# Optimization experiments

Hardware: AMD Instinct MI355X
Metric: run time of the kernel (lower is better)

The kernel has to match this reference:

```python
import math
import jax
import jax.numpy as jnp
import numpy as np
from jax import lax

B, IC, OC, K, STYLE_DIM, H, W = 16, 512, 512, 3, 512, 32, 32
EPS = 1e-8


def _blur_kernel():
    # make_kernel([1,3,3,1]) outer product, normalized, times upsample_factor**2 (=4)
    k = jnp.array([1.0, 3.0, 3.0, 1.0], dtype=jnp.float32)
    k2 = k[None, :] * k[:, None]
    k2 = k2 / k2.sum()
    return k2 * 4.0  # [4,4]


def setup_inputs() -> dict:
    key = jax.random.key(0)
    k1, k2, k3, k4 = jax.random.split(key, 4)
    return {
        "input": jax.random.normal(k1, (B, IC, H, W), dtype=jnp.float32),
        "style": jax.random.normal(k2, (B, STYLE_DIM), dtype=jnp.float32),
        "weight": jax.random.normal(k3, (1, OC, IC, K, K), dtype=jnp.float32),
        "mod_weight": jax.random.normal(k4, (IC, STYLE_DIM), dtype=jnp.float32),
        "mod_bias": jnp.ones((IC,), dtype=jnp.float32),  # bias_init=1
    }


def reference(input, style, weight, mod_weight, mod_bias):
    batch, in_ch, h, w_sp = input.shape
    out_ch, ksz = weight.shape[1], weight.shape[3]

    # EqualLinear modulation: scale = 1/sqrt(style_dim), lr_mul=1, no activation
    mod_scale = 1.0 / math.sqrt(mod_weight.shape[1])
    s = style @ (mod_weight * mod_scale).T + mod_bias  # [B, IC]

    # modulate + demodulate
    conv_scale = 1.0 / math.sqrt(in_ch * ksz * ksz)
    wmod = conv_scale * weight * s[:, None, :, None, None]  # [B, OC, IC, K, K]
    demod = lax.rsqrt(jnp.sum(wmod * wmod, axis=(2, 3, 4)) + EPS)  # [B, OC]
    wmod = wmod * demod[:, :, None, None, None]

    # conv_transpose2d(stride=2, padding=0, groups=batch) == per-sample conv with
    # lhs_dilation=2, full padding (K-1), spatially flipped kernel in OIHW layout.
    w_conv = wmod[:, :, :, ::-1, ::-1]  # [B, OC, IC, K, K]

    def one_sample(x, wk):
        # x: [IC, H, W], wk: [OC, IC, K, K] -> [OC, 2H+K-2+1, ...] (65x65 here)
        return lax.conv_general_dilated(
            x[None], wk, window_strides=(1, 1),
            padding=[(ksz - 1, ksz - 1)] * 2,
            lhs_dilation=(2, 2),
            dimension_numbers=("NCHW", "OIHW", "NCHW"))[0]

    out = jax.vmap(one_sample)(input, w_conv)  # [B, OC, 65, 65]

    # Blur: upfirdn2d(up=1, down=1, pad=(1,1)) with symmetric 4x4 kernel -> depthwise conv
    bk = _blur_kernel()
    out = jnp.pad(out, ((0, 0), (0, 0), (1, 1), (1, 1)))
    dk = jnp.tile(bk[None, None], (out_ch, 1, 1, 1))  # [OC, 1, 4, 4]
    out = lax.conv_general_dilated(
        out, dk, window_strides=(1, 1), padding="VALID",
        feature_group_count=out_ch,
        dimension_numbers=("NCHW", "OIHW", "NCHW"))  # [B, OC, 64, 64]
    return out
```

## Files before the change

kernel.cpp:

```cpp
#include <hip/hip_runtime.h>
#include <stdint.h>

typedef unsigned int uint32;
typedef unsigned short u16;
typedef short short8 __attribute__((ext_vector_type(8)));
typedef float floatx4 __attribute__((ext_vector_type(4)));

#define OFF_S      0u
#define OFF_DS     32768u
#define OFF_WSUM   65536u
#define OFF_WPACK  1114112u
#define OFF_XST    5832704u
#define OFF_U      22609920u

__device__ __forceinline__ u16 f2bf(float x){
    uint32 u = __float_as_uint(x);
    uint32 r = (u + 0x7FFFu + ((u>>16)&1u)) >> 16;
    return (u16)r;
}
__device__ __forceinline__ float bf2f(u16 h){
    return __uint_as_float(((uint32)h)<<16);
}

#define GLL16(gp, lp) \
    __builtin_amdgcn_global_load_lds( \
        (const __attribute__((address_space(1))) void*)(gp), \
        (__attribute__((address_space(3))) void*)(lp), 16, 0, 0)

__global__ __launch_bounds__(256) void k_style(const float* __restrict__ style,
                                               const float* __restrict__ mw,
                                               const float* __restrict__ mb,
                                               float* __restrict__ s){
    int gid = blockIdx.x*4 + (threadIdx.x>>6);
    int lane = threadIdx.x & 63;
    int b = gid>>9, ic = gid & 511;
    const float* sp = style + b*512;
    const float* wp = mw + (size_t)ic*512;
    float acc = 0.f;
    for (int d=lane; d<512; d+=64) acc += sp[d]*wp[d];
    for (int off=32; off; off>>=1) acc += __shfl_down(acc, off, 64);
    if (lane==0) s[b*512+ic] = acc*0.044194173824159216f + mb[ic];
}

__global__ __launch_bounds__(256) void k_wprep(const float* __restrict__ w,
                                               float* __restrict__ wsum,
                                               u16* __restrict__ wp){
    int idx = blockIdx.x*256 + threadIdx.x;
    const float* p = w + (size_t)idx*9;
    float vv[9]; float a = 0.f;
    #pragma unroll
    for (int t=0;t<9;++t){ float v=p[t]; vv[t]=v; a += v*v; }
    wsum[idx] = a;
    #pragma unroll
    for (int t=0;t<9;++t) wp[(size_t)t*262144 + idx] = f2bf(vv[t]);
}

__global__ __launch_bounds__(256) void k_dscale(const float* __restrict__ s,
                                                const float* __restrict__ wsum,
                                                float* __restrict__ ds){
    int gid = blockIdx.x*4 + (threadIdx.x>>6);
    int lane = threadIdx.x & 63;
    int b = gid>>9, oc = gid & 511;
    const float* sp = s + b*512;
    const float* wp = wsum + (size_t)oc*512;
    float acc=0.f;
    for (int d=lane; d<512; d+=64){ float sv = sp[d]; acc += sv*sv*wp[d]; }
    for (int off=32; off; off>>=1) acc += __shfl_down(acc, off, 64);
    if (lane==0){
        const float cs = 0.014731391274719738f;
        ds[b*512+oc] = cs * rsqrtf(cs*cs*acc + 1e-8f);
    }
}

__global__ __launch_bounds__(256) void k_xst(const float* __restrict__ in,
                                             const float* __restrict__ s,
                                             u16* __restrict__ xst){
    int bx = blockIdx.x;
    int b = bx>>5, i = bx&31;
    __shared__ u16 tr[32*520];
    int tid = threadIdx.x;
    int j = tid & 31;
    for (int ic = tid>>5; ic < 512; ic += 8){
        float v = in[((size_t)(b*512+ic)*32 + i)*32 + j] * s[b*512+ic];
        tr[j*520 + ic] = f2bf(v);
    }
    __syncthreads();
    for (int v = tid; v < 2048; v += 256){
        int jj = v>>6, ic8 = (v&63)*8;
        *(uint4*)(xst + (size_t)(b*1024 + i*32 + jj)*512 + ic8) =
            *(const uint4*)(&tr[jj*520 + ic8]);
    }
}

__global__ __launch_bounds__(512, 2) void k_gemm(const u16* __restrict__ A,
                                                 const u16* __restrict__ Bx,
                                                 u16* __restrict__ C,
                                                 int Ncols){
    int cpx = gridDim.x >> 3;
    int bid = blockIdx.x;
    int swz = (bid & 7)*cpx + (bid >> 3);
    int bx = swz / 18;
    int by = swz - bx*18;
    int m0 = by*256, n0 = bx*256;

    int tid = threadIdx.x;
    int lane = tid & 63;
    int w  = tid >> 6;
    int wm = w >> 2, wn = w & 3;
    int np = lane & 15, qq = lane >> 4;

    __shared__ __align__(16) char smem[131072];

    int c1 = tid,      r1 = c1 >> 2, s1 = c1 & 3, g1 = s1 ^ ((r1 >> 1) & 3);
    int c2 = tid + 512, r2 = c2 >> 2, s2 = c2 & 3, g2 = s2 ^ ((r2 >> 1) & 3);
    const u16* srcA1 = A  + (size_t)(m0 + r1)*512 + g1*8;
    const u16* srcA2 = A  + (size_t)(m0 + r2)*512 + g2*8;
    const u16* srcB1 = Bx + (size_t)(n0 + r1)*512 + g1*8;
    const u16* srcB2 = Bx + (size_t)(n0 + r2)*512 + g2*8;
    int offA1 = (tid & ~63)*8;
    int offA2 = offA1 + 4096;

    #define STAGE(T) do{ \
        u16* _b = (u16*)smem + ((T)&3)*16384; \
        GLL16(srcA1 + (size_t)(T)*32, _b + offA1); \
        GLL16(srcA2 + (size_t)(T)*32, _b + offA2); \
        GLL16(srcB1 + (size_t)(T)*32, _b + 8192 + offA1); \
        GLL16(srcB2 + (size_t)(T)*32, _b + 8192 + offA2); \
    }while(0)

    int sA = (qq ^ ((np >> 1) & 3)) * 8;
    int pAoff = (wm*128 + np)*32 + sA;
    int pBoff = (wn*64  + np)*32 + sA;

    floatx4 acc[8][4] = {};

    STAGE(0); STAGE(1); STAGE(2);
    asm volatile("s_waitcnt vmcnt(8)" ::: "memory");
    __builtin_amdgcn_s_barrier();

    #pragma unroll
    for (int t = 0; t < 16; ++t){
        const u16* base = (const u16*)smem + (t & 3)*16384;
        short8 af[8], bfr[4];
        #pragma unroll
        for (int mf = 0; mf < 8; ++mf)
            af[mf] = *(const short8*)(base + pAoff + mf*512);
        #pragma unroll
        for (int nf = 0; nf < 4; ++nf)
            bfr[nf] = *(const short8*)(base + 8192 + pBoff + nf*512);

        if (t < 13) STAGE(t+3);

        __builtin_amdgcn_s_setprio(1);
        #pragma unroll
        for (int mf = 0; mf < 8; ++mf)
            #pragma unroll
            for (int nf = 0; nf < 4; ++nf)
                acc[mf][nf] = __builtin_amdgcn_mfma_f32_16x16x32_bf16(
                    af[mf], bfr[nf], acc[mf][nf], 0,0,0);
        __builtin_amdgcn_s_setprio(0);

        if      (t < 13)  asm volatile("s_waitcnt vmcnt(8)" ::: "memory");
        else if (t == 13) asm volatile("s_waitcnt vmcnt(4)" ::: "memory");
        else if (t == 14) asm volatile("s_waitcnt vmcnt(0)" ::: "memory");
        __builtin_amdgcn_s_barrier();
    }
    #undef STAGE

    u16* Csm = (u16*)smem;
    #pragma unroll
    for (int mf = 0; mf < 8; ++mf){
        int row0 = wm*128 + mf*16 + qq*4;
        #pragma unroll
        for (int nf = 0; nf < 4; ++nf){
            int col = wn*64 + nf*16 + np;
            #pragma unroll
            for (int reg = 0; reg < 4; ++reg)
                Csm[(row0+reg)*256 + col] = f2bf(acc[mf][nf][reg]);
        }
    }
    __syncthreads();
    #pragma unroll
    for (int i = 0; i < 16; ++i){
        int c = tid + i*512;
        int row = c >> 5, cc = c & 31;
        uint4 v = *(const uint4*)(&Csm[row*256 + cc*8]);
        *(uint4*)(C + (size_t)(m0+row)*Ncols + n0 + cc*8) = v;
    }
}

__global__ __launch_bounds__(256) void k_blur2(const u16* __restrict__ U,
                                               const float* __restrict__ ds,
                                               float* __restrict__ out,
                                               int b0, int Ncols){
    int oc = blockIdx.x;
    int bp = blockIdx.y;
    int b  = b0 + bp;
    __shared__ __align__(16) u16 Usm[9*1024];
    __shared__ __align__(16) u16 HRsm[3*32*64];
    int tid = threadIdx.x;

    const u16* src0 = U + (size_t)oc*Ncols + (size_t)bp*1024;
    size_t tapstride = (size_t)512 * Ncols;
    #pragma unroll
    for (int it = 0; it < 5; ++it){
        int i = tid + it*256;
        if (i < 1152){
            int tap = i>>7, c8 = i & 127;
            *(uint4*)(&Usm[tap*1024 + c8*8]) =
                *(const uint4*)(src0 + tap*tapstride + c8*8);
        }
    }
    __syncthreads();

    #pragma unroll
    for (int it = 0; it < 12; ++it){
        int task = tid + it*256;
        int a = task >> 10, rem = task & 1023;
        int i = rem >> 5, u = rem & 31;
        const u16* base = Usm + a*3072 + i*32;
        float u0  = bf2f(base[u]);
        float u1  = bf2f(base[1024 + u]);
        float u2  = bf2f(base[2048 + u]);
        float u0p = (u < 31) ? bf2f(base[u + 1])        : 0.f;
        float u1m = (u > 0)  ? bf2f(base[1024 + u - 1]) : 0.f;
        float u1p = (u < 31) ? bf2f(base[1024 + u + 1]) : 0.f;
        float u2m = (u > 0)  ? bf2f(base[2048 + u - 1]) : 0.f;
        float HRe = u1m + 3.f*(u0 + u2m + u1) + u0p + u2;
        float HRo = u0 + u2m + 3.f*(u1 + u0p + u2) + u1p;
        uint32 packed = (uint32)f2bf(HRe) | ((uint32)f2bf(HRo) << 16);
        *(uint32*)(&HRsm[(a*32 + i)*64 + 2*u]) = packed;
    }
    __syncthreads();

    float dsc = ds[b*512 + oc] * (1.f/16.f);
    float* op = out + (size_t)(b*512 + oc) * 4096;
    #pragma unroll
    for (int it = 0; it < 4; ++it){
        int task = tid + it*256;
        int Y = task >> 4, X0 = (task & 15) * 4;
        float o0=0.f,o1=0.f,o2=0.f,o3=0.f;
        int v = Y >> 1;
        #define ACCROW(aa, ii, ww) do{ \
            int _i = (ii); \
            if ((unsigned)_i < 32u){ \
                uint2 rv = *(const uint2*)(&HRsm[((aa)*32 + _i)*64 + X0]); \
                o0 += (ww)*__uint_as_float((rv.x & 0xffffu) << 16); \
                o1 += (ww)*__uint_as_float(rv.x & 0xffff0000u); \
                o2 += (ww)*__uint_as_float((rv.y & 0xffffu) << 16); \
                o3 += (ww)*__uint_as_float(rv.y & 0xffff0000u); \
            } }while(0)
        if ((Y & 1) == 0){
            ACCROW(1, v-1, 1.f);
            ACCROW(0, v,   3.f);
            ACCROW(2, v-1, 3.f);
            ACCROW(1, v,   3.f);
            ACCROW(0, v+1, 1.f);
            ACCROW(2, v,   1.f);
        } else {
            ACCROW(0, v,   1.f);
            ACCROW(2, v-1, 1.f);
            ACCROW(1, v,   3.f);
            ACCROW(0, v+1, 3.f);
            ACCROW(2, v,   3.f);
            ACCROW(1, v+1, 1.f);
        }
        #undef ACCROW
        float4 res = make_float4(dsc*o0, dsc*o1, dsc*o2, dsc*o3);
        *(float4*)(op + Y*64 + X0) = res;
    }
}

extern "C" void kernel_launch(void* const* d_in, const int* in_sizes, int n_in,
                              void* d_out, int out_size, void* d_ws, size_t ws_size,
                              hipStream_t stream){
    const float* input  = (const float*)d_in[0];
    const float* style  = (const float*)d_in[1];
    const float* weight = (const float*)d_in[2];
    const float* mw     = (const float*)d_in[3];
    const float* mb     = (const float*)d_in[4];
    float* out = (float*)d_out;
    char* ws = (char*)d_ws;
    float* s     = (float*)(ws + OFF_S);
    float* ds    = (float*)(ws + OFF_DS);
    float* wsum  = (float*)(ws + OFF_WSUM);
    u16*   wpack = (u16*)(ws + OFF_WPACK);
    u16*   xst   = (u16*)(ws + OFF_XST);
    u16*   U     = (u16*)(ws + OFF_U);

    int NB;
    if      (ws_size >= (size_t)OFF_U + (size_t)4608*16384*2) NB = 16;
    else if (ws_size >= (size_t)OFF_U + (size_t)4608*8192*2)  NB = 8;
    else                                                       NB = 4;
    int npass = 16 / NB;
    int Ncols = NB * 1024;
    int nTilesN = Ncols / 256;

    k_style <<<2048, 256, 0, stream>>>(style, mw, mb, s);
    k_wprep <<<1024, 256, 0, stream>>>(weight, wsum, wpack);
    k_dscale<<<2048, 256, 0, stream>>>(s, wsum, ds);
    k_xst   <<<512,  256, 0, stream>>>(input, s, xst);

    for (int p = 0; p < npass; ++p){
        const u16* xp = xst + (size_t)p * NB * 1024 * 512;
        k_gemm <<<dim3(18*nTilesN), 512, 0, stream>>>(wpack, xp, U, Ncols);
        k_blur2<<<dim3(512, NB),       256, 0, stream>>>(U, ds, out, p*NB, Ncols);
    }
}
```

Baseline: 338.2 us.

## Rework LDS swizzle for GEMM tiles and pack epilogue rows into 32-bit stores

Changes the shared-memory layout of the staged A/B tiles to a row-pair XOR swizzle over 8 slots, so fragment reads and async global-to-LDS writes avoid bank conflicts. Moves the next-stage prefetch ahead of the fragment loads, so global loads are issued earlier in each iteration. Rewrites the epilogue to pack pairs of rows into 32-bit LDS words with a rotating column offset, then unpacks them into two 8-byte global stores per chunk. The aim is lower LDS conflict stalls; the cost is more index arithmetic and narrower global stores in the epilogue.

```diff
diff --git a/kernel.cpp b/kernel.cpp
--- a/kernel.cpp
+++ b/kernel.cpp
@@ -111,12 +111,14 @@
 
     __shared__ __align__(16) char smem[131072];
 
-    int c1 = tid,      r1 = c1 >> 2, s1 = c1 & 3, g1 = s1 ^ ((r1 >> 1) & 3);
-    int c2 = tid + 512, r2 = c2 >> 2, s2 = c2 & 3, g2 = s2 ^ ((r2 >> 1) & 3);
+    int rp1 = tid >> 3, sl1 = tid & 7;
+    int v1 = sl1 ^ (rp1 & 7);
+    int r1 = rp1*2 + ((v1 >> 2) & 1);
+    int g1 = v1 & 3;
     const u16* srcA1 = A  + (size_t)(m0 + r1)*512 + g1*8;
-    const u16* srcA2 = A  + (size_t)(m0 + r2)*512 + g2*8;
+    const u16* srcA2 = srcA1 + (size_t)128*512;
     const u16* srcB1 = Bx + (size_t)(n0 + r1)*512 + g1*8;
-    const u16* srcB2 = Bx + (size_t)(n0 + r2)*512 + g2*8;
+    const u16* srcB2 = srcB1 + (size_t)128*512;
     int offA1 = (tid & ~63)*8;
     int offA2 = offA1 + 4096;
 
@@ -128,9 +130,10 @@
         GLL16(srcB2 + (size_t)(T)*32, _b + 8192 + offA2); \
     }while(0)
 
-    int sA = (qq ^ ((np >> 1) & 3)) * 8;
-    int pAoff = (wm*128 + np)*32 + sA;
-    int pBoff = (wn*64  + np)*32 + sA;
+    int rpn = np >> 1;
+    int slA = ((qq + ((np & 1) << 2)) ^ rpn) << 3;
+    int pAoff = (wm*64 + rpn)*64 + slA;
+    int pBoff = (wn*32 + rpn)*64 + slA;
 
     floatx4 acc[8][4] = {};
 
@@ -140,6 +143,8 @@
 
     #pragma unroll
     for (int t = 0; t < 16; ++t){
+        if (t < 13) STAGE(t+3);
+
         const u16* base = (const u16*)smem + (t & 3)*16384;
         short8 af[8], bfr[4];
         #pragma unroll
@@ -149,8 +154,6 @@
         for (int nf = 0; nf < 4; ++nf)
             bfr[nf] = *(const short8*)(base + 8192 + pBoff + nf*512);
 
-        if (t < 13) STAGE(t+3);
-
         __builtin_amdgcn_s_setprio(1);
         #pragma unroll
         for (int mf = 0; mf < 8; ++mf)
@@ -167,25 +170,37 @@
     }
     #undef STAGE
 
-    u16* Csm = (u16*)smem;
+    uint32* Csm32 = (uint32*)smem;
     #pragma unroll
     for (int mf = 0; mf < 8; ++mf){
-        int row0 = wm*128 + mf*16 + qq*4;
         #pragma unroll
         for (int nf = 0; nf < 4; ++nf){
             int col = wn*64 + nf*16 + np;
             #pragma unroll
-            for (int reg = 0; reg < 4; ++reg)
-                Csm[(row0+reg)*256 + col] = f2bf(acc[mf][nf][reg]);
+            for (int h = 0; h < 2; ++h){
+                int rp = wm*64 + mf*8 + qq*2 + h;
+                uint32 v = (uint32)f2bf(acc[mf][nf][2*h]) |
+                           ((uint32)f2bf(acc[mf][nf][2*h+1]) << 16);
+                Csm32[rp*256 + ((col + rp*8) & 255)] = v;
+            }
         }
     }
     __syncthreads();
     #pragma unroll
     for (int i = 0; i < 16; ++i){
         int c = tid + i*512;
-        int row = c >> 5, cc = c & 31;
-        uint4 v = *(const uint4*)(&Csm[row*256 + cc*8]);
-        *(uint4*)(C + (size_t)(m0+row)*Ncols + n0 + cc*8) = v;
+        int rp = c >> 6;
+        int pc = (c & 63) * 4;
+        uint4 v = *(const uint4*)(&Csm32[rp*256 + pc]);
+        int lcol = (pc - rp*8) & 255;
+        u16* dst = C + (size_t)(m0 + rp*2)*Ncols + n0 + lcol;
+        uint2 e, o;
+        e.x = (v.x & 0xffffu) | (v.y << 16);
+        e.y = (v.z & 0xffffu) | (v.w << 16);
+        o.x = (v.x >> 16)     | (v.y & 0xffff0000u);
+        o.y = (v.z >> 16)     | (v.w & 0xffff0000u);
+        *(uint2*)(dst) = e;
+        *(uint2*)(dst + Ncols) = o;
     }
 }
 
```

New measurement: 339.4 us. No clear change (+0.4%).
